# Kernel tuning notes

Measured on AMD Instinct MI355X. Metric: run time of the kernel, lower is better.

## Reference

```python
import jax, jax.numpy as jnp
import numpy as np
from jax import lax

KERNEL_SIZE = 3
SMOOTH_NR = 0.0
SMOOTH_DR = 1e-5


def _box_sum(x, k):
    # 3D box-filter sum with zero padding (matches F.conv3d padding=(k-1)//2),
    # x: [B, C, H, W, D]. 'SAME' padding with odd k and stride 1 == symmetric pad (k-1)//2.
    return lax.reduce_window(x, jnp.array(0.0, x.dtype), lax.add,
                             window_dimensions=(1, 1, k, k, k),
                             window_strides=(1, 1, 1, 1, 1),
                             padding='SAME')


def setup_inputs() -> dict:
    key = jax.random.key(0)
    k1, k2 = jax.random.split(key)
    shape = (2, 1, 192, 192, 192)
    pred = jax.random.uniform(k1, shape, dtype=jnp.float32)
    target = jax.random.uniform(k2, shape, dtype=jnp.float32)
    return {"pred": pred, "target": target}


def reference(pred, target):
    k = KERNEL_SIZE
    kvol = float(k ** 3)
    # Local means of I, J, I^2, J^2, I*J (box filter divided by kernel volume,
    # mirroring the torch code's avg_filt grouped conv over the 5C-channel interm).
    mI = _box_sum(pred, k) / kvol
    mJ = _box_sum(target, k) / kvol
    mII = _box_sum(pred * pred, k) / kvol
    mJJ = _box_sum(target * target, k) / kvol
    mIJ = _box_sum(pred * target, k) / kvol
    # Fused NCC reduction (cc3d_fwd_interm_v1): convert means back to
    # windowed sums-based cross/variance terms using kernel_vol.
    cross = kvol * (mIJ - mI * mJ)
    p_var = kvol * (mII - mI * mI)
    t_var = kvol * (mJJ - mJ * mJ)
    ncc = (cross * cross + SMOOTH_NR) / (t_var * p_var + SMOOTH_DR)
    # reduction='mean', loss is negated squared local ZNCC
    return -jnp.mean(ncc)
```

## Files before the change

### kernel.cpp

```cpp
#include <hip/hip_runtime.h>

#define DIMB 2
#define DIMS 192
#define DPT 4
#define TX 16
#define TY 16
#define HCHUNK 6
#define ROWF 72
#define ARR_F 432
#define SLAB_F 1024

#define GLOAD_LDS16(gp, lp) __builtin_amdgcn_global_load_lds( \
    (const __attribute__((address_space(1))) void*)(gp),      \
    (__attribute__((address_space(3))) void*)(lp), 16, 0, 0)

#define WAITV(n) asm volatile("s_waitcnt vmcnt(" #n ")" ::: "memory")
#define LGKM0    asm volatile("s_waitcnt lgkmcnt(0)" ::: "memory")

__device__ __forceinline__ float dpp_left(float x) {
    const int i = __float_as_int(x);
    return __int_as_float(__builtin_amdgcn_update_dpp(i, i, 0x111, 0xf, 0xf, false));
}
__device__ __forceinline__ float dpp_right(float x) {
    const int i = __float_as_int(x);
    return __int_as_float(__builtin_amdgcn_update_dpp(i, i, 0x101, 0xf, 0xf, false));
}

__device__ __forceinline__ float ncc_row3(const float (&Pm)[5][DPT],
                                          const float (&Pc)[5][DPT],
                                          const float (&Pn)[5][DPT])
{
    const float inv = 1.0f / 27.0f;
    float acc = 0.f;
#pragma unroll
    for (int j = 0; j < DPT; ++j) {
        const float sI  = Pm[0][j] + Pc[0][j] + Pn[0][j];
        const float sJ  = Pm[1][j] + Pc[1][j] + Pn[1][j];
        const float sII = Pm[2][j] + Pc[2][j] + Pn[2][j];
        const float sJJ = Pm[3][j] + Pc[3][j] + Pn[3][j];
        const float sIJ = Pm[4][j] + Pc[4][j] + Pn[4][j];
        const float uI = sI * inv;
        const float uJ = sJ * inv;
        const float cross = sIJ - uI * sJ;
        const float pvar  = sII - uI * sI;
        const float tvar  = sJJ - uJ * sJ;
        acc += (cross * cross) * __builtin_amdgcn_rcpf(tvar * pvar + 1e-5f);
    }
    return acc;
}

__global__ __launch_bounds__(256)
void FusedLocalNormalizedCrossCorrelationLoss_37838661877790_kernel(
    const float* __restrict__ pred, const float* __restrict__ targ,
    double* __restrict__ acc_out)
{
    __shared__ float L[4][2][SLAB_F];

    const int tx = threadIdx.x, ty = threadIdx.y;
    const int tid = ty * TX + tx;
    const int lane = tid & 63, wv = tid >> 6;
    const int tyw = ty & 3;
    const int d0b = blockIdx.x * (TX * DPT);
    const int w0  = blockIdx.y * TY;
    const int bz  = blockIdx.z;
    const int b   = bz >> 5;
    const int h0  = (bz & 31) * HCHUNK;

    int co[4]; const float* ab[4];
#pragma unroll
    for (int c = 0; c < 4; ++c) {
        const int fi = c * 256 + lane * 4;
        const int a  = (fi >= ARR_F) ? 1 : 0;
        int fi2 = fi - a * ARR_F;
        if (fi2 > ARR_F - 4) fi2 = ARR_F - 4;
        const int r = fi2 / ROWF, cl = fi2 % ROWF;
        int gd = d0b - 4 + cl;
        gd = gd < 0 ? 0 : (gd > DIMS - 4 ? DIMS - 4 : gd);
        int wr = w0 - 1 + 4 * wv + r;
        wr = wr < 0 ? 0 : (wr > DIMS - 1 ? DIMS - 1 : wr);
        co[c] = wr * DIMS + gd;
        ab[c] = a ? targ : pred;
    }

    auto stage = [&](int slot, int hh) {
        const int hhc = hh < 0 ? 0 : (hh > DIMS - 1 ? DIMS - 1 : hh);
        const size_t po = ((size_t)b * DIMS + hhc) * (DIMS * DIMS);
        float* lb = &L[wv][slot][0];
#pragma unroll
        for (int c = 0; c < 4; ++c)
            GLOAD_LDS16(ab[c] + po + co[c], lb + c * 256);
    };

    const bool lo_mask = (tx == 0)      && (blockIdx.x == 0);
    const bool hi_mask = (tx == TX - 1) && (blockIdx.x == gridDim.x - 1);
    const int rb0 = 4 * tx;

    auto plane = [&](int slot, int hh, float (&P)[5][DPT]) {
#pragma unroll
        for (int c5 = 0; c5 < 5; ++c5)
#pragma unroll
            for (int j = 0; j < DPT; ++j) P[c5][j] = 0.f;
        if (hh < 0 || hh >= DIMS) return;
        const float* Lp = &L[wv][slot][0];
        const float* Lt = Lp + ARR_F;
#pragma unroll
        for (int dw = 0; dw < 3; ++dw) {
            const int wr = w0 + ty + dw - 1;
            if (wr < 0 || wr >= DIMS) continue;
            const int rb = (tyw + dw) * ROWF + rb0;
            const float4 pm = *reinterpret_cast<const float4*>(Lp + rb + 4);
            const float4 tm = *reinterpret_cast<const float4*>(Lt + rb + 4);
            float p0 = dpp_left (pm.w);
            float p5 = dpp_right(pm.x);
            float t0 = dpp_left (tm.w);
            float t5 = dpp_right(tm.x);
            if (tx == 0)      { p0 = Lp[rb + 3]; t0 = Lt[rb + 3]; }
            if (tx == TX - 1) { p5 = Lp[rb + 8]; t5 = Lt[rb + 8]; }
            if (lo_mask) { p0 = 0.f; t0 = 0.f; }
            if (hi_mask) { p5 = 0.f; t5 = 0.f; }
            const float pv[6] = {p0, pm.x, pm.y, pm.z, pm.w, p5};
            const float tv[6] = {t0, tm.x, tm.y, tm.z, tm.w, t5};
            float pp[6], tt[6], pt[6];
#pragma unroll
            for (int k = 0; k < 6; ++k) {
                pp[k] = pv[k] * pv[k];
                tt[k] = tv[k] * tv[k];
                pt[k] = pv[k] * tv[k];
            }
#define WSUM(dst, a)                                            \
            { const float c12 = a[1] + a[2], c34 = a[3] + a[4]; \
              dst[0] += a[0] + c12; dst[1] += c12 + a[3];       \
              dst[2] += a[2] + c34; dst[3] += c34 + a[5]; }
            WSUM(P[0], pv)
            WSUM(P[1], tv)
            WSUM(P[2], pp)
            WSUM(P[3], tt)
            WSUM(P[4], pt)
#undef WSUM
        }
    };

    float PA[5][DPT], PB[5][DPT], PC[5][DPT];
    float acc = 0.f;

    stage(0, h0 - 1);
    stage(1, h0);
    WAITV(4); plane(0, h0 - 1, PA); LGKM0; stage(0, h0 + 1);
    WAITV(4); plane(1, h0,     PB); LGKM0; stage(1, h0 + 2);
    WAITV(4); plane(0, h0 + 1, PC); LGKM0; stage(0, h0 + 3);
    acc += ncc_row3(PA, PB, PC);
    WAITV(4); plane(1, h0 + 2, PA); LGKM0; stage(1, h0 + 4);
    acc += ncc_row3(PB, PC, PA);
    WAITV(4); plane(0, h0 + 3, PB); LGKM0; stage(0, h0 + 5);
    acc += ncc_row3(PC, PA, PB);
    WAITV(4); plane(1, h0 + 4, PC); LGKM0; stage(1, h0 + 6);
    acc += ncc_row3(PA, PB, PC);
    WAITV(4); plane(0, h0 + 5, PA);
    acc += ncc_row3(PB, PC, PA);
    WAITV(0); plane(1, h0 + 6, PB);
    acc += ncc_row3(PC, PA, PB);

#pragma unroll
    for (int off = 32; off > 0; off >>= 1)
        acc += __shfl_down(acc, off, 64);
    __shared__ float wacc[4];
    if ((tid & 63) == 0) wacc[tid >> 6] = acc;
    __syncthreads();
    if (tid == 0) {
        const double s = (double)wacc[0] + (double)wacc[1]
                       + (double)wacc[2] + (double)wacc[3];
        atomicAdd(acc_out, s);
    }
}

__global__ void ncc_finalize(const double* __restrict__ acc,
                             float* __restrict__ out)
{
    const double n = (double)((size_t)DIMB * DIMS * DIMS * DIMS);
    out[0] = (float)(-acc[0] / n);
}

extern "C" void kernel_launch(void* const* d_in, const int* in_sizes, int n_in,
                              void* d_out, int out_size, void* d_ws, size_t ws_size,
                              hipStream_t stream) {
    const float* pred = (const float*)d_in[0];
    const float* targ = (const float*)d_in[1];
    double* acc = (double*)d_ws;

    hipMemsetAsync(d_ws, 0, sizeof(double), stream);

    dim3 block(TX, TY, 1);
    dim3 grid(DIMS / (TX * DPT), DIMS / TY, DIMB * (DIMS / HCHUNK));
    FusedLocalNormalizedCrossCorrelationLoss_37838661877790_kernel
        <<<grid, block, 0, stream>>>(pred, targ, acc);
    ncc_finalize<<<1, 1, 0, stream>>>(acc, (float*)d_out);
}
```

Before: 155.5 us.

## Stage planes through register double-buffers instead of async global-to-LDS loads

Replaces the direct global-to-LDS async loads, which double-buffered two LDS slots per wave, with float4 global loads into two register buffers. Each buffer is written into a single per-wave LDS slab just before that plane is consumed. This drops the manual vmcnt/lgkmcnt waits and halves shared memory per block, which could allow more resident blocks. In exchange it costs extra VGPRs for the staging registers plus explicit LDS store instructions, and the overlap now depends on how the compiler schedules the waits.

```diff
diff --git a/kernel.cpp b/kernel.cpp
--- a/kernel.cpp
+++ b/kernel.cpp
@@ -9,13 +9,6 @@
 #define ROWF 72
 #define ARR_F 432
 #define SLAB_F 1024
-
-#define GLOAD_LDS16(gp, lp) __builtin_amdgcn_global_load_lds( \
-    (const __attribute__((address_space(1))) void*)(gp),      \
-    (__attribute__((address_space(3))) void*)(lp), 16, 0, 0)
-
-#define WAITV(n) asm volatile("s_waitcnt vmcnt(" #n ")" ::: "memory")
-#define LGKM0    asm volatile("s_waitcnt lgkmcnt(0)" ::: "memory")
 
 __device__ __forceinline__ float dpp_left(float x) {
     const int i = __float_as_int(x);
@@ -54,7 +47,7 @@
     const float* __restrict__ pred, const float* __restrict__ targ,
     double* __restrict__ acc_out)
 {
-    __shared__ float L[4][2][SLAB_F];
+    __shared__ float L[4][SLAB_F];
 
     const int tx = threadIdx.x, ty = threadIdx.y;
     const int tid = ty * TX + tx;
@@ -82,27 +75,35 @@
         ab[c] = a ? targ : pred;
     }
 
-    auto stage = [&](int slot, int hh) {
+    float* const slab = &L[wv][0];
+    float* const wp   = slab + lane * 4;
+
+    float4 RA[4], RB[4];
+    auto loadg = [&](float4 (&R)[4], int hh) {
         const int hhc = hh < 0 ? 0 : (hh > DIMS - 1 ? DIMS - 1 : hh);
         const size_t po = ((size_t)b * DIMS + hhc) * (DIMS * DIMS);
-        float* lb = &L[wv][slot][0];
 #pragma unroll
         for (int c = 0; c < 4; ++c)
-            GLOAD_LDS16(ab[c] + po + co[c], lb + c * 256);
+            R[c] = *reinterpret_cast<const float4*>(ab[c] + po + co[c]);
+    };
+    auto put = [&](float4 (&R)[4]) {
+#pragma unroll
+        for (int c = 0; c < 4; ++c)
+            *reinterpret_cast<float4*>(wp + c * 256) = R[c];
     };
 
     const bool lo_mask = (tx == 0)      && (blockIdx.x == 0);
     const bool hi_mask = (tx == TX - 1) && (blockIdx.x == gridDim.x - 1);
     const int rb0 = 4 * tx;
 
-    auto plane = [&](int slot, int hh, float (&P)[5][DPT]) {
+    auto plane = [&](int hh, float (&P)[5][DPT]) {
 #pragma unroll
         for (int c5 = 0; c5 < 5; ++c5)
 #pragma unroll
             for (int j = 0; j < DPT; ++j) P[c5][j] = 0.f;
         if (hh < 0 || hh >= DIMS) return;
-        const float* Lp = &L[wv][slot][0];
-        const float* Lt = Lp + ARR_F;
+        const float* Lp = slab;
+        const float* Lt = slab + ARR_F;
 #pragma unroll
         for (int dw = 0; dw < 3; ++dw) {
             const int wr = w0 + ty + dw - 1;
@@ -143,21 +144,21 @@
     float PA[5][DPT], PB[5][DPT], PC[5][DPT];
     float acc = 0.f;
 
-    stage(0, h0 - 1);
-    stage(1, h0);
-    WAITV(4); plane(0, h0 - 1, PA); LGKM0; stage(0, h0 + 1);
-    WAITV(4); plane(1, h0,     PB); LGKM0; stage(1, h0 + 2);
-    WAITV(4); plane(0, h0 + 1, PC); LGKM0; stage(0, h0 + 3);
+    loadg(RA, h0 - 1);
+    loadg(RB, h0);
+    put(RA); loadg(RA, h0 + 1); plane(h0 - 1, PA);
+    put(RB); loadg(RB, h0 + 2); plane(h0,     PB);
+    put(RA); loadg(RA, h0 + 3); plane(h0 + 1, PC);
     acc += ncc_row3(PA, PB, PC);
-    WAITV(4); plane(1, h0 + 2, PA); LGKM0; stage(1, h0 + 4);
+    put(RB); loadg(RB, h0 + 4); plane(h0 + 2, PA);
     acc += ncc_row3(PB, PC, PA);
-    WAITV(4); plane(0, h0 + 3, PB); LGKM0; stage(0, h0 + 5);
+    put(RA); loadg(RA, h0 + 5); plane(h0 + 3, PB);
     acc += ncc_row3(PC, PA, PB);
-    WAITV(4); plane(1, h0 + 4, PC); LGKM0; stage(1, h0 + 6);
+    put(RB); loadg(RB, h0 + 6); plane(h0 + 4, PC);
     acc += ncc_row3(PA, PB, PC);
-    WAITV(4); plane(0, h0 + 5, PA);
+    put(RA);                    plane(h0 + 5, PA);
     acc += ncc_row3(PB, PC, PA);
-    WAITV(0); plane(1, h0 + 6, PB);
+    put(RB);                    plane(h0 + 6, PB);
     acc += ncc_row3(PC, PA, PB);
 
 #pragma unroll
```

Result: slower. 258.2 us (+66.1%).
